# Kernel tuning notes

Hardware: AMD Instinct MI355X
Metric: run time of the kernel (lower is better)

Reference implementation:

```python
import math
import jax, jax.numpy as jnp
import numpy as np

BS = 4; C = 128; D = 128; NH = 4; NL = 2; NP = 8
SHAPES = [(64, 96), (32, 48)]            # (H, W) per level
STARTS = [0, SHAPES[0][0] * SHAPES[0][1]]  # level_start_index


def lrelu(x):
    return jnp.where(x >= 0, x, 0.1 * x)


def conv2d(x, w, b):
    y = jax.lax.conv_general_dilated(x, w, (1, 1), [(1, 1), (1, 1)],
                                     dimension_numbers=('NCHW', 'OIHW', 'NCHW'))
    return y + b[None, :, None, None]


def pos_enc_sine(bs, H, W, npf=64, T=10000.0):
    # DETR PositionEmbeddingSine (normalize=True), mask of ones -> cumsum = index+1
    scale = 2.0 * math.pi
    eps = 1e-6
    y = (jnp.arange(1, H + 1, dtype=jnp.float32) / (H + eps) * scale)[:, None]
    x = (jnp.arange(1, W + 1, dtype=jnp.float32) / (W + eps) * scale)[None, :]
    y = jnp.broadcast_to(y, (H, W))
    x = jnp.broadcast_to(x, (H, W))
    dim_t = T ** (2.0 * (jnp.arange(npf) // 2).astype(jnp.float32) / npf)
    px = x[..., None] / dim_t
    py = y[..., None] / dim_t
    def interleave(p):
        return jnp.stack([jnp.sin(p[..., 0::2]), jnp.cos(p[..., 1::2])], -1).reshape(H, W, npf)
    pos = jnp.concatenate([interleave(py), interleave(px)], -1)  # [H,W,2*npf]
    return jnp.broadcast_to(pos.transpose(2, 0, 1)[None], (bs, 2 * npf, H, W))


def ref_points(bs, H, W):
    ys = (jnp.arange(H, dtype=jnp.float32) + 0.5) / H
    xs = (jnp.arange(W, dtype=jnp.float32) + 0.5) / W
    gy, gx = jnp.meshgrid(ys, xs, indexing='ij')
    ref = jnp.stack([gx.reshape(-1), gy.reshape(-1)], -1)  # [hw, 2] (x, y)
    return jnp.broadcast_to(ref[None, :, None, :], (bs, H * W, 1, 2))


def sample_level(v, loc, Hl, Wl):
    # v: [bs, Hl*Wl, nh, d]; loc: [bs, nq, nh, np, 2] in [0,1] -> grid_sample bilinear, zero pad
    bs, nq, nh, npts, _ = loc.shape
    d = v.shape[-1]
    x = loc[..., 0] * Wl - 0.5
    y = loc[..., 1] * Hl - 0.5
    x0f = jnp.floor(x); y0f = jnp.floor(y)
    fx = x - x0f; fy = y - y0f
    x0 = x0f.astype(jnp.int32); y0 = y0f.astype(jnp.int32)
    def gather(xi, yi):
        valid = (xi >= 0) & (xi < Wl) & (yi >= 0) & (yi < Hl)
        idx = jnp.clip(yi, 0, Hl - 1) * Wl + jnp.clip(xi, 0, Wl - 1)  # [bs,nq,nh,np]
        idx = idx.transpose(0, 1, 3, 2).reshape(bs, nq * npts, nh)
        g = jnp.take_along_axis(v, idx[..., None], axis=1)  # [bs,nq*np,nh,d]
        g = g.reshape(bs, nq, npts, nh, d).transpose(0, 1, 3, 2, 4)  # [bs,nq,nh,np,d]
        return g * valid[..., None]
    w00 = (1 - fx) * (1 - fy); w01 = fx * (1 - fy); w10 = (1 - fx) * fy; w11 = fx * fy
    return (gather(x0, y0) * w00[..., None] + gather(x0 + 1, y0) * w01[..., None]
            + gather(x0, y0 + 1) * w10[..., None] + gather(x0 + 1, y0 + 1) * w11[..., None])


def msda(value, loc, weights):
    # value [bs,Nv,nh,d], loc [bs,nq,nh,nl,np,2], weights [bs,nq,nh,nl,np]
    out = 0.0
    for l, (Hl, Wl) in enumerate(SHAPES):
        v_l = value[:, STARTS[l]:STARTS[l] + Hl * Wl]
        s = sample_level(v_l, loc[:, :, :, l], Hl, Wl)  # [bs,nq,nh,np,d]
        out = out + jnp.einsum('bqhpd,bqhp->bqhd', s, weights[:, :, :, l])
    bs, nq, nh, d = out.shape
    return out.reshape(bs, nq, nh * d)


def block(query, value, qloc, so_w, so_b, aw_w, aw_b, op_w, op_b):
    bs, nq, _ = query.shape
    off = (query @ so_w + so_b).reshape(bs, nq, NH, NL, NP, 2)
    aw = jax.nn.softmax((query @ aw_w + aw_b).reshape(bs, nq, NH, NL * NP), -1)
    aw = aw.reshape(bs, nq, NH, NL, NP)
    norm = jnp.array([[w, h] for (h, w) in SHAPES], jnp.float32)  # [nl,2] = (W,H)
    loc = qloc[:, :, None, :, None, :] + off / norm[None, None, None, :, None, :]
    return msda(value, loc, aw) @ op_w + op_b  # dropout = identity (eval)


def _forward(feat0_l0, feat0_l1, feat1_l0, feat1_l1,
             cw1, cb1, cw2, cb2, cw3, cb3, vw, vb, lvl_emb,
             so_w0, so_b0, aw_w0, aw_b0, op_w0, op_b0,
             so_w1, so_b1, aw_w1, aw_b1, op_w1, op_b1):
    bs = feat0_l0.shape[0]
    H1, W1 = SHAPES[-1]
    # scale_conv stem on feature0_list[-1]
    q = lrelu(conv2d(feat0_l1, cw1, cb1))
    q = lrelu(conv2d(q, cw2, cb2))
    q = lrelu(conv2d(q, cw3, cb3))
    q = q + pos_enc_sine(bs, H1, W1, npf=D // 2)
    qloc = ref_points(bs, H1, W1)  # [bs, hw, 1, 2]
    # flatten levels + level embeds
    f0 = jnp.concatenate([f.reshape(bs, C, -1) + lvl_emb[l][None, :, None]
                          for l, f in enumerate([feat0_l0, feat0_l1])], axis=2)
    f1 = jnp.concatenate([f.reshape(bs, C, -1) + lvl_emb[l][None, :, None]
                          for l, f in enumerate([feat1_l0, feat1_l1])], axis=2)
    cat = jnp.concatenate([f0, f1], axis=1)  # [bs, 2C, Nv]
    value = jnp.einsum('oc,bcn->bno', vw, cat) + vb  # 1x1 Conv1d -> [bs, Nv, D]
    value = jnp.broadcast_to(value[:, :, None, :], (bs, value.shape[1], NH, D))
    query = q.reshape(bs, D, -1).transpose(0, 2, 1)  # [bs, hw, D]
    query = block(query, value, qloc, so_w0, so_b0, aw_w0, aw_b0, op_w0, op_b0)
    query = block(query, value, qloc, so_w1, so_b1, aw_w1, aw_b1, op_w1, op_b1)
    return query.reshape(bs, H1, W1, D).transpose(0, 3, 1, 2)


def setup_inputs() -> dict:
    key = jax.random.key(0)
    ks = iter(jax.random.split(key, 32))
    def rn(shape, s=1.0):
        return jax.random.normal(next(ks), shape, jnp.float32) * s
    inp = {}
    inp['feat0_l0'] = rn((BS, C, SHAPES[0][0], SHAPES[0][1]))
    inp['feat0_l1'] = rn((BS, C, SHAPES[1][0], SHAPES[1][1]))
    inp['feat1_l0'] = rn((BS, C, SHAPES[0][0], SHAPES[0][1]))
    inp['feat1_l1'] = rn((BS, C, SHAPES[1][0], SHAPES[1][1]))
    inp['cw1'] = rn((2 * D, C, 3, 3), 0.03); inp['cb1'] = rn((2 * D,), 0.01)
    inp['cw2'] = rn((D, 2 * D, 3, 3), 0.03); inp['cb2'] = rn((D,), 0.01)
    inp['cw3'] = rn((D, D, 3, 3), 0.03); inp['cb3'] = rn((D,), 0.01)
    inp['vw'] = rn((D, 2 * C), 0.05); inp['vb'] = rn((D,), 0.01)
    inp['lvl_emb'] = rn((NL, C), 0.05)
    for i in range(2):
        inp[f'so_w{i}'] = rn((D, NH * NL * NP * 2), 0.02)
        inp[f'so_b{i}'] = rn((NH * NL * NP * 2,), 0.5)
        inp[f'aw_w{i}'] = rn((D, NH * NL * NP), 0.02)
        inp[f'aw_b{i}'] = rn((NH * NL * NP,), 0.01)
        inp[f'op_w{i}'] = rn((NH * D, D), 0.05)
        inp[f'op_b{i}'] = rn((D,), 0.01)
    return inp


def reference(feat0_l0, feat0_l1, feat1_l0, feat1_l1,
              cw1, cb1, cw2, cb2, cw3, cb3, vw, vb, lvl_emb,
              so_w0, so_b0, aw_w0, aw_b0, op_w0, op_b0,
              so_w1, so_b1, aw_w1, aw_b1, op_w1, op_b1):
    return _forward(feat0_l0, feat0_l1, feat1_l0, feat1_l1,
                    cw1, cb1, cw2, cb2, cw3, cb3, vw, vb, lvl_emb,
                    so_w0, so_b0, aw_w0, aw_b0, op_w0, op_b0,
                    so_w1, so_b1, aw_w1, aw_b1, op_w1, op_b1)
```

## Files before the change

### kernel.cpp

```cpp
#include <hip/hip_runtime.h>
#include <hip/hip_bf16.h>

typedef unsigned short u16;
typedef u16   u16x8 __attribute__((ext_vector_type(8)));
typedef short s16x8 __attribute__((ext_vector_type(8)));
typedef float f32x4 __attribute__((ext_vector_type(4)));

__device__ __forceinline__ float bf2f(u16 u) {
    union { unsigned int i; float f; } v; v.i = ((unsigned int)u) << 16; return v.f;
}
__device__ __forceinline__ u16 f2bf(float f) {
    unsigned int x = __float_as_uint(f);
    return (u16)((x + 0x7fffu + ((x >> 16) & 1u)) >> 16);
}
__device__ __forceinline__ float ldv(const void* p, size_t i, int f32) {
    return f32 ? ((const float*)p)[i] : bf2f(((const u16*)p)[i]);
}

template<int ACT, int OUTM, int OUT_BF16, int BN>
__device__ __forceinline__ void gemm_body(
    u16* __restrict__ smem, int bid,
    const u16* __restrict__ A, const u16* __restrict__ Bt,
    const u16* __restrict__ bias, void* __restrict__ Cv,
    int M, int K, int ldc, int nbase, const int* __restrict__ flag)
{
    constexpr int NF = BN >> 4;
    u16 (*As)[72] = (u16(*)[72])smem;
    u16 (*Bs)[72] = (u16(*)[72])(smem + 4608);

    const int t    = threadIdx.x;
    const int wv   = t >> 6, lane = t & 63;
    const int fr   = lane & 15, fg = lane >> 4;
    const int tiles_m = M >> 6;
    const int bm = bid % tiles_m, bn = bid / tiles_m;
    const int m0 = bm << 6, n0 = bn * BN;

    f32x4 acc[NF] = {};
    const int srow = t >> 2;
    const int scol = (t & 3) << 4;
    const int brow = (BN == 64) ? srow : (t >> 3);
    const int bcol = (BN == 64) ? scol : ((t & 7) << 3);
    const u16* Ap = A  + (size_t)(m0 + srow) * K + scol;
    const u16* Bp = Bt + (size_t)(n0 + brow) * K + bcol;

    const int ns = K >> 6;
    uint4 av0 = *(const uint4*)Ap, av1 = *(const uint4*)(Ap + 8);
    uint4 bv0 = *(const uint4*)Bp, bv1 = {0,0,0,0};
    if constexpr (BN == 64) bv1 = *(const uint4*)(Bp + 8);
    for (int s = 0; s < ns; ++s) {
        __syncthreads();
        *(uint4*)&As[srow][scol]     = av0;  *(uint4*)&As[srow][scol + 8] = av1;
        *(uint4*)&Bs[brow][bcol]     = bv0;
        if constexpr (BN == 64) *(uint4*)&Bs[brow][bcol + 8] = bv1;
        __syncthreads();
        if (s + 1 < ns) {
            const u16* An = Ap + ((s + 1) << 6);
            const u16* Bn = Bp + ((s + 1) << 6);
            av0 = *(const uint4*)An;  av1 = *(const uint4*)(An + 8);
            bv0 = *(const uint4*)Bn;
            if constexpr (BN == 64) bv1 = *(const uint4*)(Bn + 8);
        }
        union U { uint4 q; s16x8 v; };
        #pragma unroll
        for (int kk = 0; kk < 2; ++kk) {
            U af; af.q = *(const uint4*)&As[(wv << 4) + fr][(kk << 5) + (fg << 3)];
            U bf[NF];
            #pragma unroll
            for (int j = 0; j < NF; ++j)
                bf[j].q = *(const uint4*)&Bs[(j << 4) + fr][(kk << 5) + (fg << 3)];
            #pragma unroll
            for (int j = 0; j < NF; ++j)
                acc[j] = __builtin_amdgcn_mfma_f32_16x16x32_bf16(af.v, bf[j].v, acc[j], 0, 0, 0);
        }
    }

    float vv[NF][4];
    #pragma unroll
    for (int r = 0; r < 4; ++r) {
        float bvv = bf2f(bias[m0 + (wv << 4) + (fg << 2) + r]);
        #pragma unroll
        for (int j = 0; j < NF; ++j) {
            float v = acc[j][r] + bvv;
            if (ACT) v = (v >= 0.f) ? v : 0.1f * v;
            vv[j][r] = v;
        }
    }

    if constexpr (OUTM == 0) {
        #pragma unroll
        for (int j = 0; j < NF; ++j)
            #pragma unroll
            for (int r = 0; r < 4; ++r) {
                size_t idx = (size_t)(m0 + (wv << 4) + (fg << 2) + r) * ldc
                           + (nbase + n0 + (j << 4) + fr);
                if (OUT_BF16) ((u16*)Cv)[idx] = f2bf(vv[j][r]);
                else          ((float*)Cv)[idx] = vv[j][r];
            }
    } else if constexpr (OUTM == 1) {
        __syncthreads();
        u16* bb = smem;
        #pragma unroll
        for (int j = 0; j < NF; ++j)
            #pragma unroll
            for (int r = 0; r < 4; ++r)
                bb[((j << 4) + fr) * 72 + (wv << 4) + (fg << 2) + r] = f2bf(vv[j][r]);
        __syncthreads();
        if constexpr (BN == 64) {
            int row = t >> 2, seg = (t & 3) << 4;
            const uint4* src = (const uint4*)&bb[row * 72 + seg];
            uint4* dst = (uint4*)((u16*)Cv + (size_t)(nbase + n0 + row) * M + m0 + seg);
            dst[0] = src[0];
            dst[1] = src[1];
        } else {
            int row = t >> 3, seg = (t & 7) << 3;
            const uint4* src = (const uint4*)&bb[row * 72 + seg];
            uint4* dst = (uint4*)((u16*)Cv + (size_t)(nbase + n0 + row) * M + m0 + seg);
            dst[0] = src[0];
        }
    } else {
        __syncthreads();
        constexpr int LDB = BN + 8;
        u16* bb = smem;
        #pragma unroll
        for (int j = 0; j < NF; ++j)
            #pragma unroll
            for (int r = 0; r < 4; ++r)
                bb[((wv << 4) + (fg << 2) + r) * LDB + (j << 4) + fr] = f2bf(vv[j][r]);
        __syncthreads();
        int f32o = *flag;
        constexpr int EPT = BN / 4;
        int mrow = t >> 2, seg = (t & 3) * EPT;
        int b = n0 / 1536, hw0 = (n0 % 1536) + seg;
        size_t base = (size_t)(b * 128 + m0 + mrow) * 1536 + hw0;
        if (!f32o) {
            #pragma unroll
            for (int q = 0; q < EPT / 8; ++q)
                *(uint4*)((u16*)Cv + base + q * 8) = *(const uint4*)&bb[mrow * LDB + seg + q * 8];
        } else {
            float* dst = (float*)Cv + base;
            #pragma unroll
            for (int j = 0; j < EPT; ++j) dst[j] = bf2f(bb[mrow * LDB + seg + j]);
        }
    }
}

template<int CIN, int POS, int BN>
__device__ __forceinline__ void conv_body(
    u16* __restrict__ smem, int bid,
    const u16* __restrict__ A, const u16* __restrict__ X,
    const u16* __restrict__ bias, u16* __restrict__ Cv, int M)
{
    constexpr int NF = BN >> 4;
    u16 (*As)[72] = (u16(*)[72])smem;
    u16 (*Bs)[72] = (u16(*)[72])(smem + 4608);

    constexpr int NK2 = CIN / 64;
    constexpr int TOT = 9 * NK2;

    const int t    = threadIdx.x;
    const int wv   = t >> 6, lane = t & 63;
    const int fr   = lane & 15, fg = lane >> 4;
    const int tiles_m = M >> 6;
    const int bm = bid % tiles_m, bn = bid / tiles_m;
    const int m0 = bm << 6, n0 = bn * BN;

    const int srow = t >> 2;
    const int scol = (t & 3) << 4;
    const int brow = (BN == 64) ? srow : (t >> 3);
    const int bcol = (BN == 64) ? scol : ((t & 7) << 3);
    const int n  = n0 + brow;
    const int hw = n % 1536;
    const int hp = hw / 48, wp = hw % 48;
    const u16* Ar = A + (size_t)(m0 + srow) * (9 * CIN) + scol;

    f32x4 acc[NF] = {};

    auto ld = [&](int s, uint4& a0, uint4& a1, uint4& b0, uint4& b1) {
        int tap = s / NK2, k0 = (s % NK2) << 6;
        int dy = tap / 3 - 1, dx = tap % 3 - 1;
        bool vr = ((unsigned)(hp + dy) < 32u) && ((unsigned)(wp + dx) < 48u);
        const u16* Ap = Ar + tap * CIN + k0;
        a0 = *(const uint4*)Ap;  a1 = *(const uint4*)(Ap + 8);
        if (vr) {
            const u16* Bp = X + (size_t)(n + dy * 48 + dx) * CIN + bcol + k0;
            b0 = *(const uint4*)Bp;
            if constexpr (BN == 64) b1 = *(const uint4*)(Bp + 8);
        } else {
            b0 = uint4{0,0,0,0};  b1 = uint4{0,0,0,0};
        }
    };

    uint4 av0, av1, bv0, bv1;
    ld(0, av0, av1, bv0, bv1);
    for (int s = 0; s < TOT; ++s) {
        __syncthreads();
        *(uint4*)&As[srow][scol]     = av0;  *(uint4*)&As[srow][scol + 8] = av1;
        *(uint4*)&Bs[brow][bcol]     = bv0;
        if constexpr (BN == 64) *(uint4*)&Bs[brow][bcol + 8] = bv1;
        __syncthreads();
        if (s + 1 < TOT) ld(s + 1, av0, av1, bv0, bv1);
        union U { uint4 q; s16x8 v; };
        #pragma unroll
        for (int kk = 0; kk < 2; ++kk) {
            U af; af.q = *(const uint4*)&As[(wv << 4) + fr][(kk << 5) + (fg << 3)];
            U bf[NF];
            #pragma unroll
            for (int j = 0; j < NF; ++j)
                bf[j].q = *(const uint4*)&Bs[(j << 4) + fr][(kk << 5) + (fg << 3)];
            #pragma unroll
            for (int j = 0; j < NF; ++j)
                acc[j] = __builtin_amdgcn_mfma_f32_16x16x32_bf16(af.v, bf[j].v, acc[j], 0, 0, 0);
        }
    }

    float vv[NF][4];
    #pragma unroll
    for (int r = 0; r < 4; ++r) {
        float bvv = bf2f(bias[m0 + (wv << 4) + (fg << 2) + r]);
        #pragma unroll
        for (int j = 0; j < NF; ++j) {
            float v = acc[j][r] + bvv;
            vv[j][r] = (v >= 0.f) ? v : 0.1f * v;
        }
    }

    if (POS) {
        const float TWO_PI = 6.283185307179586f;
        #pragma unroll
        for (int j = 0; j < NF; ++j) {
            int ntok = n0 + (j << 4) + fr;
            int hw2 = ntok % 1536;
            int hp2 = hw2 / 48, wp2 = hw2 % 48;
            float yv = (float)(hp2 + 1) * (TWO_PI / (32.f + 1e-6f));
            float xv = (float)(wp2 + 1) * (TWO_PI / (48.f + 1e-6f));
            #pragma unroll
            for (int r = 0; r < 4; ++r) {
                int d = m0 + (wv << 4) + (fg << 2) + r;
                int mm = (d & 63) >> 1;
                float dim = exp2f((float)mm * (13.287712379549449f / 32.f));
                float val = ((d < 64) ? yv : xv) / dim;
                vv[j][r] += (d & 1) ? cosf(val) : sinf(val);
            }
        }
    }

    __syncthreads();
    u16* bb = smem;
    #pragma unroll
    for (int j = 0; j < NF; ++j)
        #pragma unroll
        for (int r = 0; r < 4; ++r)
            bb[((j << 4) + fr) * 72 + (wv << 4) + (fg << 2) + r] = f2bf(vv[j][r]);
    __syncthreads();
    if constexpr (BN == 64) {
        int row = t >> 2, seg = (t & 3) << 4;
        const uint4* src = (const uint4*)&bb[row * 72 + seg];
        uint4* dst = (uint4*)(Cv + (size_t)(n0 + row) * M + m0 + seg);
        dst[0] = src[0];
        dst[1] = src[1];
    } else {
        int row = t >> 3, seg = (t & 7) << 3;
        const uint4* src = (const uint4*)&bb[row * 72 + seg];
        uint4* dst = (uint4*)(Cv + (size_t)(n0 + row) * M + m0 + seg);
        dst[0] = src[0];
    }
}

template<int ACT, int OUTM, int OUT_BF16, int BN>
__global__ __launch_bounds__(256) void gemm_kn(
    const u16* __restrict__ A, const u16* __restrict__ Bt,
    const u16* __restrict__ bias, void* __restrict__ Cv,
    int M, int K, int ldc, int nbase, const int* __restrict__ flag)
{
    __shared__ __align__(16) u16 smem[9216];
    gemm_body<ACT, OUTM, OUT_BF16, BN>(smem, blockIdx.x, A, Bt, bias, Cv, M, K, ldc, nbase, flag);
}

template<int CIN, int POS, int BN>
__global__ __launch_bounds__(256) void conv_gemm(
    const u16* __restrict__ A, const u16* __restrict__ X,
    const u16* __restrict__ bias, u16* __restrict__ Cv, int M)
{
    __shared__ __align__(16) u16 smem[9216];
    conv_body<CIN, POS, BN>(smem, blockIdx.x, A, X, bias, Cv, M);
}

__global__ __launch_bounds__(256) void val_conv1_k(
    const u16* __restrict__ AVW, const u16* __restrict__ CATT,
    const u16* __restrict__ vb, u16* __restrict__ VAL,
    const u16* __restrict__ AW1, const u16* __restrict__ X0,
    const u16* __restrict__ cb1, u16* __restrict__ CH1)
{
    __shared__ __align__(16) u16 smem[9216];
    int bid = blockIdx.x;
    if (bid < 960) gemm_body<0, 1, 1, 64>(smem, bid, AVW, CATT, vb, VAL, 128, 256, 0, 0, nullptr);
    else           conv_body<128, 0, 64>(smem, bid - 960, AW1, X0, cb1, CH1, 256);
}

struct P21 { const void* p[21]; };

__global__ __launch_bounds__(256) void prep_fused(
    P21 a, const void* __restrict__ f00, const void* __restrict__ f01,
    const void* __restrict__ f10, const void* __restrict__ f11,
    int* __restrict__ FLAG,
    u16* AW1, u16* AW2, u16* AW3, u16* AVW,
    u16* APJ0, u16* APJ1, u16* AOP0, u16* AOP1,
    u16* BPJ0, u16* BPJ1, u16* SB,
    u16* CATT, u16* X0)
{
    __shared__ __align__(16) u16 Ts[128 * 66];
    const int t = threadIdx.x;
    unsigned int w = ((const unsigned int*)f00)[t];
    float pa = fabsf(bf2f((u16)(w & 0xFFFFu)));
    int cnt = __syncthreads_count(pa > 1e-6f && pa < 1e4f);
    const int f32 = (cnt < 128);
    const int bid = blockIdx.x;
    if (bid == 0 && t == 0) *FLAG = f32;

    if (bid < 3718) {
        int g = bid * 256 + t;
        if (g < 294912) { int m = g / 1152, rem = g % 1152, tap = rem >> 7, ci = rem & 127;
            AW1[g] = f2bf(ldv(a.p[0], (size_t)m * 1152 + ci * 9 + tap, f32)); return; }
        g -= 294912;
        if (g < 294912) { int m = g / 2304, rem = g % 2304, tap = rem >> 8, ci = rem & 255;
            AW2[g] = f2bf(ldv(a.p[2], (size_t)m * 2304 + ci * 9 + tap, f32)); return; }
        g -= 294912;
        if (g < 147456) { int m = g / 1152, rem = g % 1152, tap = rem >> 7, ci = rem & 127;
            AW3[g] = f2bf(ldv(a.p[4], (size_t)m * 1152 + ci * 9 + tap, f32)); return; }
        g -= 147456;
        if (g < 32768) { AVW[g] = f2bf(ldv(a.p[6], g, f32)); return; }
        g -= 32768;
        if (g < 24576) { int o = g >> 7, d = g & 127;
            APJ0[g] = f2bf(o < 128 ? ldv(a.p[9], d * 128 + o, f32)
                                   : ldv(a.p[11], d * 64 + (o - 128), f32)); return; }
        g -= 24576;
        if (g < 24576) { int o = g >> 7, d = g & 127;
            APJ1[g] = f2bf(o < 128 ? ldv(a.p[15], d * 128 + o, f32)
                                   : ldv(a.p[17], d * 64 + (o - 128), f32)); return; }
        g -= 24576;
        if (g < 65536) { int o = g >> 9, k = g & 511; AOP0[g] = f2bf(ldv(a.p[13], k * 128 + o, f32)); return; }
        g -= 65536;
        if (g < 65536) { int o = g >> 9, k = g & 511; AOP1[g] = f2bf(ldv(a.p[19], k * 128 + o, f32)); return; }
        g -= 65536;
        if (g < 192) { BPJ0[g] = f2bf(g < 128 ? ldv(a.p[10], g, f32) : ldv(a.p[12], g - 128, f32)); return; }
        g -= 192;
        if (g < 192) { BPJ1[g] = f2bf(g < 128 ? ldv(a.p[16], g, f32) : ldv(a.p[18], g - 128, f32)); return; }
        g -= 192;
        if (g < 1152) {
            const int off[8] = {0, 256, 384, 512, 640, 896, 1024, 1152};
            const int src[7] = {1, 3, 5, 7, 8, 14, 20};
            int s = 0;
            #pragma unroll
            for (int i = 1; i < 7; ++i) s += (g >= off[i]);
            SB[g] = f2bf(ldv(a.p[src[s]], g - off[s], f32));
        }
        return;
    }

    const void* src; u16* dst;
    int b, hw0, HW, rowlen, coloff, lvl, addemb;
    if (bid < 4678) {
        int g = bid - 3718;
        int half = g & 1;  g >>= 1;
        b = g / 120;  int tile = g % 120;
        lvl = (tile >= 96) ? 1 : 0;
        int tl = lvl ? tile - 96 : tile;
        hw0 = tl << 6;
        HW = lvl ? 1536 : 6144;
        src = (half == 0) ? (lvl ? f01 : f00) : (lvl ? f11 : f10);
        dst = CATT + (size_t)(b * 7680 + lvl * 6144 + hw0) * 256;
        rowlen = 256; coloff = half << 7; addemb = 1;
    } else {
        int g = bid - 4678;
        b = g / 24;  hw0 = (g % 24) << 6;
        HW = 1536; src = f01;
        dst = X0 + (size_t)(b * 1536 + hw0) * 128;
        rowlen = 128; coloff = 0; lvl = 1; addemb = 0;
    }

    {
        int c = t >> 1, hseg = (t & 1) << 5;
        size_t base = (size_t)(b * 128 + c) * HW + hw0 + hseg;
        u16* dstl = &Ts[c * 66 + hseg];
        if (!f32) {
            const u16* s8 = (const u16*)src + base;
            *(uint4*)(dstl)      = *(const uint4*)(s8);
            *(uint4*)(dstl + 8)  = *(const uint4*)(s8 + 8);
            *(uint4*)(dstl + 16) = *(const uint4*)(s8 + 16);
            *(uint4*)(dstl + 24) = *(const uint4*)(s8 + 24);
        } else {
            const float* sf = (const float*)src + base;
            #pragma unroll
            for (int q = 0; q < 32; ++q) dstl[q] = f2bf(sf[q]);
        }
    }
    __syncthreads();
    {
        int tok = t & 63, cseg = (t >> 6) << 5;
        u16 outv[32];
        #pragma unroll
        for (int j = 0; j < 32; ++j) {
            float x = bf2f(Ts[(cseg + j) * 66 + tok]);
            if (addemb) x += ldv(a.p[8], lvl * 128 + cseg + j, f32);
            outv[j] = f2bf(x);
        }
        u16* drow = dst + (size_t)tok * rowlen + coloff + cseg;
        #pragma unroll
        for (int q = 0; q < 4; ++q)
            *(uint4*)(drow + q * 8) = *(const uint4*)(&outv[q * 8]);
    }
}

__global__ void msda_sample(const float* __restrict__ PA, const u16* __restrict__ VAL,
                            u16* __restrict__ S)
{
    __shared__ int   SMI[4][64];
    __shared__ float SMW[4][64];
    __shared__ float LG[64];
    __shared__ float EW[64];
    int bid = blockIdx.x;
    int tok = ((bid & 7) * 768) + (bid >> 3);
    int t = threadIdx.x;
    int b = tok / 1536, hw = tok % 1536;
    int hp = hw / 48, wp = hw % 48;

    if (t < 64) {
        int l = (t >> 3) & 1, p = t & 7, h = t >> 4;
        int orow = h * 32 + l * 16 + p * 2;
        float offx = PA[(size_t)orow * 6144 + tok];
        float offy = PA[(size_t)(orow + 1) * 6144 + tok];
        LG[t]      = PA[(size_t)(128 + h * 16 + l * 8 + p) * 6144 + tok];
        float Wl = l ? 48.f : 96.f, Hl = l ? 32.f : 64.f;
        int iWl = l ? 48 : 96, iHl = l ? 32 : 64;
        int base = l ? 6144 : 0;
        float locx = (wp + 0.5f) / 48.f + offx / Wl;
        float locy = (hp + 0.5f) / 32.f + offy / Hl;
        float x = locx * Wl - 0.5f;
        float y = locy * Hl - 0.5f;
        float xf = floorf(x), yf = floorf(y);
        float fx = x - xf, fy = y - yf;
        int ix = (int)xf, iy = (int)yf;
        int vrow = b * 7680 + base;
        float w00 = (1.f - fx) * (1.f - fy), w01 = fx * (1.f - fy);
        float w10 = (1.f - fx) * fy,         w11 = fx * fy;
        bool vx0 = (ix >= 0) & (ix < iWl),     vx1 = (ix + 1 >= 0) & (ix + 1 < iWl);
        bool vy0 = (iy >= 0) & (iy < iHl),     vy1 = (iy + 1 >= 0) & (iy + 1 < iHl);
        SMI[0][t] = (vx0 & vy0) ? vrow + iy * iWl + ix           : 0;
        SMI[1][t] = (vx1 & vy0) ? vrow + iy * iWl + ix + 1       : 0;
        SMI[2][t] = (vx0 & vy1) ? vrow + (iy + 1) * iWl + ix     : 0;
        SMI[3][t] = (vx1 & vy1) ? vrow + (iy + 1) * iWl + ix + 1 : 0;
        SMW[0][t] = (vx0 & vy0) ? w00 : 0.f;
        SMW[1][t] = (vx1 & vy0) ? w01 : 0.f;
        SMW[2][t] = (vx0 & vy1) ? w10 : 0.f;
        SMW[3][t] = (vx1 & vy1) ? w11 : 0.f;
    }
    __syncthreads();
    if (t < 64) {
        int h0 = t & ~15;
        float mx = -1e30f;
        for (int i = 0; i < 16; ++i) mx = fmaxf(mx, LG[h0 + i]);
        EW[t] = expf(LG[t] - mx);
    }
    __syncthreads();
    if (t < 64) {
        int h0 = t & ~15;
        float s = 0.f;
        for (int i = 0; i < 16; ++i) s += EW[h0 + i];
        float aw = EW[t] / s;
        SMW[0][t] *= aw; SMW[1][t] *= aw; SMW[2][t] *= aw; SMW[3][t] *= aw;
    }
    __syncthreads();

    const int h = t >> 5, sub = t & 31, dseg = sub & 15, half = sub >> 4;
    const u16* Vb = VAL + (size_t)dseg * 8;
    float acc[8] = {0.f, 0.f, 0.f, 0.f, 0.f, 0.f, 0.f, 0.f};
    #pragma unroll
    for (int rr = 0; rr < 32; rr += 16) {
        u16x8 vreg[16];
        float wreg[16];
        #pragma unroll
        for (int q = 0; q < 16; ++q) {
            int pr = (half << 5) + rr + q;
            int s = pr >> 2, c = pr & 3;
            wreg[q] = SMW[c][(h << 4) + s];
            vreg[q] = *(const u16x8*)(Vb + (size_t)SMI[c][(h << 4) + s] * 128);
        }
        #pragma unroll
        for (int q = 0; q < 16; ++q)
            #pragma unroll
            for (int j = 0; j < 8; ++j) acc[j] += wreg[q] * bf2f(vreg[q][j]);
    }
    #pragma unroll
    for (int j = 0; j < 8; ++j) acc[j] += __shfl_xor(acc[j], 16, 64);
    if (!half) {
        u16x8 o;
        #pragma unroll
        for (int j = 0; j < 8; ++j) o[j] = f2bf(acc[j]);
        *(u16x8*)(S + (size_t)tok * 512 + (h << 7) + (dseg << 3)) = o;
    }
}

extern "C" void kernel_launch(void* const* d_in, const int* in_sizes, int n_in,
                              void* d_out, int out_size, void* d_ws, size_t ws_size,
                              hipStream_t stream)
{
    (void)in_sizes; (void)n_in; (void)out_size; (void)ws_size;

    char* ws = (char*)d_ws;
    size_t off = 0;
    auto alloc = [&](size_t bytes) { size_t o = off; off += (bytes + 255) & ~(size_t)255; return o; };
    int*   FLAG = (int*)(ws + alloc(256));
    u16*   AW1  = (u16*)(ws + alloc(294912ull * 2));
    u16*   AW2  = (u16*)(ws + alloc(294912ull * 2));
    u16*   AW3  = (u16*)(ws + alloc(147456ull * 2));
    u16*   AVW  = (u16*)(ws + alloc(32768ull * 2));
    u16*   APJ0 = (u16*)(ws + alloc(24576ull * 2));
    u16*   APJ1 = (u16*)(ws + alloc(24576ull * 2));
    u16*   AOP0 = (u16*)(ws + alloc(65536ull * 2));
    u16*   AOP1 = (u16*)(ws + alloc(65536ull * 2));
    u16*   BPJ0 = (u16*)(ws + alloc(512));
    u16*   BPJ1 = (u16*)(ws + alloc(512));
    u16*   SB   = (u16*)(ws + alloc(1152ull * 2));
    u16*   VAL  = (u16*)(ws + alloc(30720ull * 128 * 2));
    u16*   X0   = (u16*)(ws + alloc(6144ull * 128 * 2));
    u16*   CH1  = (u16*)(ws + alloc(6144ull * 256 * 2));
    u16*   CH2  = (u16*)(ws + alloc(6144ull * 128 * 2));
    u16*   QT0  = (u16*)(ws + alloc(6144ull * 128 * 2));
    u16*   QT1  = (u16*)(ws + alloc(6144ull * 128 * 2));
    char*  R    = ws + alloc(30720ull * 256 * 2);
    u16*   CATT = (u16*)R;
    float* PA   = (float*)R;
    u16*   S    = (u16*)(R + 192ull * 6144 * 4);

    u16* cb1C = SB + 0;   u16* cb2C = SB + 256;  u16* cb3C = SB + 384;
    u16* vbC  = SB + 512;
    u16* ob0C = SB + 896; u16* ob1C = SB + 1024;

    P21 a;
    const int widx[21] = {4,5,6,7,8,9,10,11,12, 13,14,15,16,17,18, 19,20,21,22,23,24};
    for (int i = 0; i < 21; ++i) a.p[i] = d_in[widx[i]];

    prep_fused<<<4774, 256, 0, stream>>>(a, d_in[0], d_in[1], d_in[2], d_in[3], FLAG,
                                         AW1, AW2, AW3, AVW,
                                         APJ0, APJ1, AOP0, AOP1, BPJ0, BPJ1, SB,
                                         CATT, X0);

    val_conv1_k<<<960 + 384, 256, 0, stream>>>(AVW, CATT, vbC, VAL, AW1, X0, cb1C, CH1);

    conv_gemm<256, 0, 32><<<2 * 192, 256, 0, stream>>>(AW2, CH1, cb2C, CH2, 128);
    conv_gemm<128, 1, 32><<<2 * 192, 256, 0, stream>>>(AW3, CH2, cb3C, QT0, 128);

    gemm_kn<0, 0, 0, 32><<<3 * 192, 256, 0, stream>>>(APJ0, QT0, BPJ0, PA, 192, 128, 6144, 0, FLAG);
    msda_sample<<<6144, 128, 0, stream>>>(PA, VAL, S);
    gemm_kn<0, 1, 1, 32><<<2 * 192, 256, 0, stream>>>(AOP0, S, ob0C, QT1, 128, 512, 0, 0, FLAG);

    gemm_kn<0, 0, 0, 32><<<3 * 192, 256, 0, stream>>>(APJ1, QT1, BPJ1, PA, 192, 128, 6144, 0, FLAG);
    msda_sample<<<6144, 128, 0, stream>>>(PA, VAL, S);
    gemm_kn<0, 2, 1, 32><<<2 * 192, 256, 0, stream>>>(AOP1, S, ob1C, d_out, 128, 512, 0, 0, FLAG);
}
```

Baseline: 143.6 us.

## Fold layer-0 output projection into layer-1 offset/attention projection GEMM

The layer-0 output projection (op_w0) and the layer-1 sampling-offset/attention-weight projection are both linear with nothing between them. They are now composed into a single 192x512 weight W1 = APJ1·OPW0 and a bias B1, computed inside the val_conv1 launch. This removes one GEMM launch and the QT1 intermediate round trip. The trade-off is a K=512 GEMM in place of K=128, plus extra precomputation and one more bf16 rounding step in the composed weight; a few minor cleanups (flag read only when needed, unsigned bound checks) ride along.

```diff
diff --git a/kernel.cpp b/kernel.cpp
--- a/kernel.cpp
+++ b/kernel.cpp
@@ -16,13 +16,24 @@
 __device__ __forceinline__ float ldv(const void* p, size_t i, int f32) {
     return f32 ? ((const float*)p)[i] : bf2f(((const u16*)p)[i]);
 }
+
+struct P21 { const void* p[21]; };
+
+struct Args {
+    P21 a;
+    const void *f00, *f01, *f10, *f11;
+    u16 *AW1, *AW2, *AW3, *AVW, *APJ0, *APJ1, *AOP1, *BPJ0, *BPJ1, *SB;
+    u16 *OPW0, *ZB, *W1, *B1;
+    u16 *CATT, *X0, *VAL, *CH1, *CH2, *QT0, *S;
+    float* PA;
+};
 
 template<int ACT, int OUTM, int OUT_BF16, int BN>
 __device__ __forceinline__ void gemm_body(
     u16* __restrict__ smem, int bid,
     const u16* __restrict__ A, const u16* __restrict__ Bt,
     const u16* __restrict__ bias, void* __restrict__ Cv,
-    int M, int K, int ldc, int nbase, const int* __restrict__ flag)
+    int M, int K, int ldc, int nbase, int f32o)
 {
     constexpr int NF = BN >> 4;
     u16 (*As)[72] = (u16(*)[72])smem;
@@ -127,7 +138,6 @@
             for (int r = 0; r < 4; ++r)
                 bb[((wv << 4) + (fg << 2) + r) * LDB + (j << 4) + fr] = f2bf(vv[j][r]);
         __syncthreads();
-        int f32o = *flag;
         constexpr int EPT = BN / 4;
         int mrow = t >> 2, seg = (t & 3) * EPT;
         int b = n0 / 1536, hw0 = (n0 % 1536) + seg;
@@ -273,7 +283,8 @@
     int M, int K, int ldc, int nbase, const int* __restrict__ flag)
 {
     __shared__ __align__(16) u16 smem[9216];
-    gemm_body<ACT, OUTM, OUT_BF16, BN>(smem, blockIdx.x, A, Bt, bias, Cv, M, K, ldc, nbase, flag);
+    int f32o = (OUTM == 2) ? *flag : 0;
+    gemm_body<ACT, OUTM, OUT_BF16, BN>(smem, blockIdx.x, A, Bt, bias, Cv, M, K, ldc, nbase, f32o);
 }
 
 template<int CIN, int POS, int BN>
@@ -285,96 +296,102 @@
     conv_body<CIN, POS, BN>(smem, blockIdx.x, A, X, bias, Cv, M);
 }
 
-__global__ __launch_bounds__(256) void val_conv1_k(
-    const u16* __restrict__ AVW, const u16* __restrict__ CATT,
-    const u16* __restrict__ vb, u16* __restrict__ VAL,
-    const u16* __restrict__ AW1, const u16* __restrict__ X0,
-    const u16* __restrict__ cb1, u16* __restrict__ CH1)
+__global__ __launch_bounds__(256) void val_conv1_k(Args g)
 {
     __shared__ __align__(16) u16 smem[9216];
     int bid = blockIdx.x;
-    if (bid < 960) gemm_body<0, 1, 1, 64>(smem, bid, AVW, CATT, vb, VAL, 128, 256, 0, 0, nullptr);
-    else           conv_body<128, 0, 64>(smem, bid - 960, AW1, X0, cb1, CH1, 256);
-}
-
-struct P21 { const void* p[21]; };
-
-__global__ __launch_bounds__(256) void prep_fused(
-    P21 a, const void* __restrict__ f00, const void* __restrict__ f01,
-    const void* __restrict__ f10, const void* __restrict__ f11,
-    int* __restrict__ FLAG,
-    u16* AW1, u16* AW2, u16* AW3, u16* AVW,
-    u16* APJ0, u16* APJ1, u16* AOP0, u16* AOP1,
-    u16* BPJ0, u16* BPJ1, u16* SB,
-    u16* CATT, u16* X0)
+    u16* cb1 = g.SB;
+    u16* vb  = g.SB + 512;
+    u16* ob0 = g.SB + 896;
+    if (bid < 960) {
+        gemm_body<0, 1, 1, 64>(smem, bid, g.AVW, g.CATT, vb, g.VAL, 128, 256, 0, 0, 0);
+    } else if (bid < 1344) {
+        conv_body<128, 0, 64>(smem, bid - 960, g.AW1, g.X0, cb1, g.CH1, 256);
+    } else if (bid < 1392) {
+        gemm_body<0, 0, 1, 32>(smem, bid - 1344, g.APJ1, g.OPW0, g.ZB, g.W1, 192, 128, 512, 0, 0);
+    } else {
+        int m = threadIdx.x;
+        if (m < 192) {
+            float s = bf2f(g.BPJ1[m]);
+            const u16* row = g.APJ1 + (size_t)m * 128;
+            for (int k = 0; k < 128; ++k) s += bf2f(row[k]) * bf2f(ob0[k]);
+            g.B1[m] = f2bf(s);
+        }
+    }
+}
+
+__global__ __launch_bounds__(256) void prep_fused(Args g, int* __restrict__ FLAG)
 {
     __shared__ __align__(16) u16 Ts[128 * 66];
     const int t = threadIdx.x;
-    unsigned int w = ((const unsigned int*)f00)[t];
+    const P21& a = g.a;
+    unsigned int w = ((const unsigned int*)g.f00)[t];
     float pa = fabsf(bf2f((u16)(w & 0xFFFFu)));
     int cnt = __syncthreads_count(pa > 1e-6f && pa < 1e4f);
     const int f32 = (cnt < 128);
     const int bid = blockIdx.x;
     if (bid == 0 && t == 0) *FLAG = f32;
 
-    if (bid < 3718) {
-        int g = bid * 256 + t;
-        if (g < 294912) { int m = g / 1152, rem = g % 1152, tap = rem >> 7, ci = rem & 127;
-            AW1[g] = f2bf(ldv(a.p[0], (size_t)m * 1152 + ci * 9 + tap, f32)); return; }
-        g -= 294912;
-        if (g < 294912) { int m = g / 2304, rem = g % 2304, tap = rem >> 8, ci = rem & 255;
-            AW2[g] = f2bf(ldv(a.p[2], (size_t)m * 2304 + ci * 9 + tap, f32)); return; }
-        g -= 294912;
-        if (g < 147456) { int m = g / 1152, rem = g % 1152, tap = rem >> 7, ci = rem & 127;
-            AW3[g] = f2bf(ldv(a.p[4], (size_t)m * 1152 + ci * 9 + tap, f32)); return; }
-        g -= 147456;
-        if (g < 32768) { AVW[g] = f2bf(ldv(a.p[6], g, f32)); return; }
-        g -= 32768;
-        if (g < 24576) { int o = g >> 7, d = g & 127;
-            APJ0[g] = f2bf(o < 128 ? ldv(a.p[9], d * 128 + o, f32)
-                                   : ldv(a.p[11], d * 64 + (o - 128), f32)); return; }
-        g -= 24576;
-        if (g < 24576) { int o = g >> 7, d = g & 127;
-            APJ1[g] = f2bf(o < 128 ? ldv(a.p[15], d * 128 + o, f32)
-                                   : ldv(a.p[17], d * 64 + (o - 128), f32)); return; }
-        g -= 24576;
-        if (g < 65536) { int o = g >> 9, k = g & 511; AOP0[g] = f2bf(ldv(a.p[13], k * 128 + o, f32)); return; }
-        g -= 65536;
-        if (g < 65536) { int o = g >> 9, k = g & 511; AOP1[g] = f2bf(ldv(a.p[19], k * 128 + o, f32)); return; }
-        g -= 65536;
-        if (g < 192) { BPJ0[g] = f2bf(g < 128 ? ldv(a.p[10], g, f32) : ldv(a.p[12], g - 128, f32)); return; }
-        g -= 192;
-        if (g < 192) { BPJ1[g] = f2bf(g < 128 ? ldv(a.p[16], g, f32) : ldv(a.p[18], g - 128, f32)); return; }
-        g -= 192;
-        if (g < 1152) {
+    if (bid < 3975) {
+        int gg = bid * 256 + t;
+        if (gg < 294912) { int m = gg / 1152, rem = gg % 1152, tap = rem >> 7, ci = rem & 127;
+            g.AW1[gg] = f2bf(ldv(a.p[0], (size_t)m * 1152 + ci * 9 + tap, f32)); return; }
+        gg -= 294912;
+        if (gg < 294912) { int m = gg / 2304, rem = gg % 2304, tap = rem >> 8, ci = rem & 255;
+            g.AW2[gg] = f2bf(ldv(a.p[2], (size_t)m * 2304 + ci * 9 + tap, f32)); return; }
+        gg -= 294912;
+        if (gg < 147456) { int m = gg / 1152, rem = gg % 1152, tap = rem >> 7, ci = rem & 127;
+            g.AW3[gg] = f2bf(ldv(a.p[4], (size_t)m * 1152 + ci * 9 + tap, f32)); return; }
+        gg -= 147456;
+        if (gg < 32768) { g.AVW[gg] = f2bf(ldv(a.p[6], gg, f32)); return; }
+        gg -= 32768;
+        if (gg < 24576) { int o = gg >> 7, d = gg & 127;
+            g.APJ0[gg] = f2bf(o < 128 ? ldv(a.p[9], d * 128 + o, f32)
+                                      : ldv(a.p[11], d * 64 + (o - 128), f32)); return; }
+        gg -= 24576;
+        if (gg < 24576) { int o = gg >> 7, d = gg & 127;
+            g.APJ1[gg] = f2bf(o < 128 ? ldv(a.p[15], d * 128 + o, f32)
+                                      : ldv(a.p[17], d * 64 + (o - 128), f32)); return; }
+        gg -= 24576;
+        if (gg < 65536) { int o = gg >> 9, k = gg & 511; g.AOP1[gg] = f2bf(ldv(a.p[19], k * 128 + o, f32)); return; }
+        gg -= 65536;
+        if (gg < 192) { g.BPJ0[gg] = f2bf(gg < 128 ? ldv(a.p[10], gg, f32) : ldv(a.p[12], gg - 128, f32)); return; }
+        gg -= 192;
+        if (gg < 192) { g.BPJ1[gg] = f2bf(gg < 128 ? ldv(a.p[16], gg, f32) : ldv(a.p[18], gg - 128, f32)); return; }
+        gg -= 192;
+        if (gg < 1152) {
             const int off[8] = {0, 256, 384, 512, 640, 896, 1024, 1152};
             const int src[7] = {1, 3, 5, 7, 8, 14, 20};
             int s = 0;
             #pragma unroll
-            for (int i = 1; i < 7; ++i) s += (g >= off[i]);
-            SB[g] = f2bf(ldv(a.p[src[s]], g - off[s], f32));
-        }
+            for (int i = 1; i < 7; ++i) s += (gg >= off[i]);
+            g.SB[gg] = f2bf(ldv(a.p[src[s]], gg - off[s], f32)); return;
+        }
+        gg -= 1152;
+        if (gg < 65536) { g.OPW0[gg] = f2bf(ldv(a.p[13], gg, f32)); return; }
+        gg -= 65536;
+        if (gg < 192) { g.ZB[gg] = 0; return; }
         return;
     }
 
     const void* src; u16* dst;
     int b, hw0, HW, rowlen, coloff, lvl, addemb;
-    if (bid < 4678) {
-        int g = bid - 3718;
-        int half = g & 1;  g >>= 1;
-        b = g / 120;  int tile = g % 120;
+    if (bid < 4935) {
+        int gg = bid - 3975;
+        int half = gg & 1;  gg >>= 1;
+        b = gg / 120;  int tile = gg % 120;
         lvl = (tile >= 96) ? 1 : 0;
         int tl = lvl ? tile - 96 : tile;
         hw0 = tl << 6;
         HW = lvl ? 1536 : 6144;
-        src = (half == 0) ? (lvl ? f01 : f00) : (lvl ? f11 : f10);
-        dst = CATT + (size_t)(b * 7680 + lvl * 6144 + hw0) * 256;
+        src = (half == 0) ? (lvl ? g.f01 : g.f00) : (lvl ? g.f11 : g.f10);
+        dst = g.CATT + (size_t)(b * 7680 + lvl * 6144 + hw0) * 256;
         rowlen = 256; coloff = half << 7; addemb = 1;
     } else {
-        int g = bid - 4678;
-        b = g / 24;  hw0 = (g % 24) << 6;
-        HW = 1536; src = f01;
-        dst = X0 + (size_t)(b * 1536 + hw0) * 128;
+        int gg = bid - 4935;
+        b = gg / 24;  hw0 = (gg % 24) << 6;
+        HW = 1536; src = g.f01;
+        dst = g.X0 + (size_t)(b * 1536 + hw0) * 128;
         rowlen = 128; coloff = 0; lvl = 1; addemb = 0;
     }
 
@@ -443,16 +460,16 @@
         int vrow = b * 7680 + base;
         float w00 = (1.f - fx) * (1.f - fy), w01 = fx * (1.f - fy);
         float w10 = (1.f - fx) * fy,         w11 = fx * fy;
-        bool vx0 = (ix >= 0) & (ix < iWl),     vx1 = (ix + 1 >= 0) & (ix + 1 < iWl);
-        bool vy0 = (iy >= 0) & (iy < iHl),     vy1 = (iy + 1 >= 0) & (iy + 1 < iHl);
-        SMI[0][t] = (vx0 & vy0) ? vrow + iy * iWl + ix           : 0;
-        SMI[1][t] = (vx1 & vy0) ? vrow + iy * iWl + ix + 1       : 0;
-        SMI[2][t] = (vx0 & vy1) ? vrow + (iy + 1) * iWl + ix     : 0;
-        SMI[3][t] = (vx1 & vy1) ? vrow + (iy + 1) * iWl + ix + 1 : 0;
-        SMW[0][t] = (vx0 & vy0) ? w00 : 0.f;
-        SMW[1][t] = (vx1 & vy0) ? w01 : 0.f;
-        SMW[2][t] = (vx0 & vy1) ? w10 : 0.f;
-        SMW[3][t] = (vx1 & vy1) ? w11 : 0.f;
+        bool vx0 = (unsigned)ix < (unsigned)iWl,       vx1 = (unsigned)(ix + 1) < (unsigned)iWl;
+        bool vy0 = (unsigned)iy < (unsigned)iHl,       vy1 = (unsigned)(iy + 1) < (unsigned)iHl;
+        SMI[0][t] = (vx0 && vy0) ? vrow + iy * iWl + ix           : 0;
+        SMI[1][t] = (vx1 && vy0) ? vrow + iy * iWl + ix + 1       : 0;
+        SMI[2][t] = (vx0 && vy1) ? vrow + (iy + 1) * iWl + ix     : 0;
+        SMI[3][t] = (vx1 && vy1) ? vrow + (iy + 1) * iWl + ix + 1 : 0;
+        SMW[0][t] = (vx0 && vy0) ? w00 : 0.f;
+        SMW[1][t] = (vx1 && vy0) ? w01 : 0.f;
+        SMW[2][t] = (vx0 && vy1) ? w10 : 0.f;
+        SMW[3][t] = (vx1 && vy1) ? w11 : 0.f;
     }
     __syncthreads();
     if (t < 64) {
@@ -464,10 +481,11 @@
     __syncthreads();
     if (t < 64) {
         int h0 = t & ~15;
-        float s = 0.f;
-        for (int i = 0; i < 16; ++i) s += EW[h0 + i];
-        float aw = EW[t] / s;
-        SMW[0][t] *= aw; SMW[1][t] *= aw; SMW[2][t] *= aw; SMW[3][t] *= aw;
+        float sum = 0.f;
+        for (int i = 0; i < 16; ++i) sum += EW[h0 + i];
+        float aw = EW[t] / sum;
+        SMW[0][t] *= aw; SMW[1][t] *= aw;
+        SMW[2][t] *= aw; SMW[3][t] *= aw;
     }
     __syncthreads();
 
@@ -516,45 +534,50 @@
     u16*   AVW  = (u16*)(ws + alloc(32768ull * 2));
     u16*   APJ0 = (u16*)(ws + alloc(24576ull * 2));
     u16*   APJ1 = (u16*)(ws + alloc(24576ull * 2));
-    u16*   AOP0 = (u16*)(ws + alloc(65536ull * 2));
     u16*   AOP1 = (u16*)(ws + alloc(65536ull * 2));
     u16*   BPJ0 = (u16*)(ws + alloc(512));
     u16*   BPJ1 = (u16*)(ws + alloc(512));
     u16*   SB   = (u16*)(ws + alloc(1152ull * 2));
+    u16*   OPW0 = (u16*)(ws + alloc(65536ull * 2));
+    u16*   ZB   = (u16*)(ws + alloc(512));
+    u16*   W1   = (u16*)(ws + alloc(98304ull * 2));
+    u16*   B1   = (u16*)(ws + alloc(512));
     u16*   VAL  = (u16*)(ws + alloc(30720ull * 128 * 2));
     u16*   X0   = (u16*)(ws + alloc(6144ull * 128 * 2));
     u16*   CH1  = (u16*)(ws + alloc(6144ull * 256 * 2));
     u16*   CH2  = (u16*)(ws + alloc(6144ull * 128 * 2));
     u16*   QT0  = (u16*)(ws + alloc(6144ull * 128 * 2));
-    u16*   QT1  = (u16*)(ws + alloc(6144ull * 128 * 2));
     char*  R    = ws + alloc(30720ull * 256 * 2);
     u16*   CATT = (u16*)R;
     float* PA   = (float*)R;
     u16*   S    = (u16*)(R + 192ull * 6144 * 4);
 
-    u16* cb1C = SB + 0;   u16* cb2C = SB + 256;  u16* cb3C = SB + 384;
-    u16* vbC  = SB + 512;
-    u16* ob0C = SB + 896; u16* ob1C = SB + 1024;
-
-    P21 a;
+    u16* cb2C = SB + 256;  u16* cb3C = SB + 384;
+    u16* ob1C = SB + 1024;
+
+    Args g;
     const int widx[21] = {4,5,6,7,8,9,10,11,12, 13,14,15,16,17,18, 19,20,21,22,23,24};
-    for (int i = 0; i < 21; ++i) a.p[i] = d_in[widx[i]];
-
-    prep_fused<<<4774, 256, 0, stream>>>(a, d_in[0], d_in[1], d_in[2], d_in[3], FLAG,
-                                         AW1, AW2, AW3, AVW,
-                                         APJ0, APJ1, AOP0, AOP1, BPJ0, BPJ1, SB,
-                                         CATT, X0);
-
-    val_conv1_k<<<960 + 384, 256, 0, stream>>>(AVW, CATT, vbC, VAL, AW1, X0, cb1C, CH1);
+    for (int i = 0; i < 21; ++i) g.a.p[i] = d_in[widx[i]];
+    g.f00 = d_in[0]; g.f01 = d_in[1]; g.f10 = d_in[2]; g.f11 = d_in[3];
+    g.AW1 = AW1; g.AW2 = AW2; g.AW3 = AW3; g.AVW = AVW;
+    g.APJ0 = APJ0; g.APJ1 = APJ1; g.AOP1 = AOP1;
+    g.BPJ0 = BPJ0; g.BPJ1 = BPJ1; g.SB = SB;
+    g.OPW0 = OPW0; g.ZB = ZB; g.W1 = W1; g.B1 = B1;
+    g.CATT = CATT; g.X0 = X0; g.VAL = VAL; g.CH1 = CH1; g.CH2 = CH2;
+    g.QT0 = QT0; g.S = S; g.PA = PA;
+
+    prep_fused<<<5031, 256, 0, stream>>>(g, FLAG);
+
+    val_conv1_k<<<1393, 256, 0, stream>>>(g);
 
     conv_gemm<256, 0, 32><<<2 * 192, 256, 0, stream>>>(AW2, CH1, cb2C, CH2, 128);
     conv_gemm<128, 1, 32><<<2 * 192, 256, 0, stream>>>(AW3, CH2, cb3C, QT0, 128);
 
     gemm_kn<0, 0, 0, 32><<<3 * 192, 256, 0, stream>>>(APJ0, QT0, BPJ0, PA, 192, 128, 6144, 0, FLAG);
     msda_sample<<<6144, 128, 0, stream>>>(PA, VAL, S);
-    gemm_kn<0, 1, 1, 32><<<2 * 192, 256, 0, stream>>>(AOP0, S, ob0C, QT1, 128, 512, 0, 0, FLAG);
-
-    gemm_kn<0, 0, 0, 32><<<3 * 192, 256, 0, stream>>>(APJ1, QT1, BPJ1, PA, 192, 128, 6144, 0, FLAG);
+
+    gemm_kn<0, 0, 0, 32><<<3 * 192, 256, 0, stream>>>(W1, S, B1, PA, 192, 512, 6144, 0, FLAG);
     msda_sample<<<6144, 128, 0, stream>>>(PA, VAL, S);
+
     gemm_kn<0, 2, 1, 32><<<2 * 192, 256, 0, stream>>>(AOP1, S, ob1C, d_out, 128, 512, 0, 0, FLAG);
 }
```

Result: no change. 142.1 us (median of 2 runs) (-1.0%).
